# Performance work log

Hardware: AMD Instinct MI355X
Metric: run time of the kernel (lower is better)

Reference implementation:

```python
import jax, jax.numpy as jnp
import numpy as np

B, MAXLEN = 256, 10000
N_ATOMS, N_BONDS, N_ANG, N_TOR = 2000, 1999, 1998, 1997
NBT, NAT, NTT = 50, 100, 200
EPS = 1e-8


def setup_inputs() -> dict:
    rng = np.random.default_rng(0)
    feats = np.zeros((B, MAXLEN, 9), np.float32)
    # col 0: atom types
    feats[:, :N_ATOMS, 0] = rng.integers(0, 20, (B, N_ATOMS))
    # col 5: flattened coords [3*N]
    coords = (rng.standard_normal((B, N_ATOMS, 3)) * 2.0).astype(np.float32)
    feats[:, :3 * N_ATOMS, 5] = coords.reshape(B, -1)
    # col 6: bonds (i, j, type) along a chain
    i = np.arange(N_BONDS, dtype=np.float32)
    bonds = np.zeros((B, N_BONDS, 3), np.float32)
    bonds[..., 0] = i; bonds[..., 1] = i + 1
    bonds[..., 2] = rng.integers(0, NBT, (B, N_BONDS))
    feats[:, :3 * N_BONDS, 6] = bonds.reshape(B, -1)
    # col 7: angles (i, j, k, type)
    a = np.arange(N_ANG, dtype=np.float32)
    angs = np.zeros((B, N_ANG, 4), np.float32)
    angs[..., 0] = a; angs[..., 1] = a + 1; angs[..., 2] = a + 2
    angs[..., 3] = rng.integers(0, NAT, (B, N_ANG))
    feats[:, :4 * N_ANG, 7] = angs.reshape(B, -1)
    # col 8: torsions (i, j, k, l, type)
    t = np.arange(N_TOR, dtype=np.float32)
    tors = np.zeros((B, N_TOR, 5), np.float32)
    tors[..., 0] = t; tors[..., 1] = t + 1; tors[..., 2] = t + 2; tors[..., 3] = t + 3
    tors[..., 4] = rng.integers(0, NTT, (B, N_TOR))
    feats[:, :5 * N_TOR, 8] = tors.reshape(B, -1)
    # per-column valid lengths
    lengths = np.zeros((B, 9), np.int32)
    lengths[:, 0] = N_ATOMS
    lengths[:, 5] = 3 * N_ATOMS
    lengths[:, 6] = 3 * N_BONDS
    lengths[:, 7] = 4 * N_ANG
    lengths[:, 8] = 5 * N_TOR
    # learned params: (k, eq_value, multiplicity) per type row
    P = NBT + NAT + NTT
    opt = np.abs(rng.standard_normal((P, 3))).astype(np.float32)
    opt[:, 2] = rng.integers(1, 4, P).astype(np.float32)
    return {
        "features": jnp.asarray(feats),
        "lengths": jnp.asarray(lengths),
        "opt_pars": jnp.asarray(opt),
        "bond_type": jnp.arange(NBT, dtype=jnp.float32),
        "angle_type": jnp.arange(NAT, dtype=jnp.float32) + NBT,
        "tor_type": jnp.arange(NTT, dtype=jnp.float32) + NBT + NAT,
    }


def _gather(coords, idx):
    # coords [B,N,3], idx [B,M] -> [B,M,3]
    return jnp.take_along_axis(
        coords, jnp.broadcast_to(idx[..., None], idx.shape + (3,)), axis=1)


def _energy(features, lengths, opt_pars, bond_map, angle_map, tor_map):
    Bn = features.shape[0]
    coords = features[:, :3 * N_ATOMS, 5].reshape(Bn, N_ATOMS, 3)
    bonds = features[:, :3 * N_BONDS, 6].reshape(Bn, N_BONDS, 3).astype(jnp.int32)
    angs = features[:, :4 * N_ANG, 7].reshape(Bn, N_ANG, 4).astype(jnp.int32)
    tors = features[:, :5 * N_TOR, 8].reshape(Bn, N_TOR, 5).astype(jnp.int32)

    # ---- bonds: harmonic E = k * (r - r0)^2 ----
    ri, rj = _gather(coords, bonds[..., 0]), _gather(coords, bonds[..., 1])
    r = jnp.sqrt(jnp.sum((ri - rj) ** 2, -1) + EPS)          # [B,NB]
    pb = opt_pars[bond_map[bonds[..., 2]]]                   # [B,NB,3]
    eb = pb[..., 0] * (r - pb[..., 1]) ** 2
    mb = jnp.arange(N_BONDS)[None, :] < (lengths[:, 6:7] // 3)
    ebonds = jnp.sum(jnp.where(mb, eb, 0.0), -1)

    # ---- angles: harmonic E = k * (theta - theta0)^2 ----
    ai, aj, ak = (_gather(coords, angs[..., c]) for c in range(3))
    u, v = ai - aj, ak - aj
    cos = jnp.sum(u * v, -1) * jax.lax.rsqrt(
        (jnp.sum(u * u, -1) + EPS) * (jnp.sum(v * v, -1) + EPS))
    theta = jnp.arccos(jnp.clip(cos, -1.0 + 1e-6, 1.0 - 1e-6))
    pa = opt_pars[angle_map[angs[..., 3]]]
    ea = pa[..., 0] * (theta - pa[..., 1]) ** 2
    ma = jnp.arange(N_ANG)[None, :] < (lengths[:, 7:8] // 4)
    eangles = jnp.sum(jnp.where(ma, ea, 0.0), -1)

    # ---- torsions: E = k * (1 + cos(n*phi - phi0)) ----
    ti, tj, tk, tl = (_gather(coords, tors[..., c]) for c in range(4))
    b1, b2, b3 = tj - ti, tk - tj, tl - tk
    n1 = jnp.cross(b1, b2)
    n2 = jnp.cross(b2, b3)
    b2h = b2 * jax.lax.rsqrt(jnp.sum(b2 * b2, -1, keepdims=True) + EPS)
    m1 = jnp.cross(n1, b2h)
    phi = jnp.arctan2(jnp.sum(m1 * n2, -1), jnp.sum(n1 * n2, -1))
    pt = opt_pars[tor_map[tors[..., 4]]]
    et = pt[..., 0] * (1.0 + jnp.cos(pt[..., 2] * phi - pt[..., 1]))
    mt = jnp.arange(N_TOR)[None, :] < (lengths[:, 8:9] // 5)
    etors = jnp.sum(jnp.where(mt, et, 0.0), -1)

    return ebonds + eangles + etors                          # [B]


def reference(features, lengths, opt_pars, bond_type, angle_type, tor_type):
    return _energy(features, lengths, opt_pars,
                   bond_type.astype(jnp.int32),
                   angle_type.astype(jnp.int32),
                   tor_type.astype(jnp.int32))
```

## Files before the change

kernel.cpp:

```cpp
#include <hip/hip_runtime.h>


#define BS 512

__global__ __launch_bounds__(BS) void energy_kernel(
    const float* __restrict__ features,
    const int*   __restrict__ lengths,
    const float* __restrict__ opt_pars,
    const float* __restrict__ bond_type,
    const float* __restrict__ angle_type,
    const float* __restrict__ tor_type,
    float*       __restrict__ out)
{
    constexpr int MAXLEN  = 10000;
    constexpr int N_ATOMS = 2000;
    constexpr int NBT = 50, NAT = 100, NTT = 200;
    constexpr float EPS = 1e-8f;

    const int b   = blockIdx.x;
    const int tid = threadIdx.x;
    const float* __restrict__ fb = features + (size_t)b * MAXLEN * 9;

    __shared__ float sc[3 * N_ATOMS];
    __shared__ float sbp[3 * NBT];
    __shared__ float sap[3 * NAT];
    __shared__ float stp[3 * NTT];
    __shared__ float swsum[BS / 64];

    for (int i = tid; i < 3 * N_ATOMS; i += BS)
        sc[i] = fb[i * 9 + 5];

    for (int i = tid; i < NBT; i += BS) {
        int idx = (int)bond_type[i];
        sbp[3*i+0] = opt_pars[3*idx+0];
        sbp[3*i+1] = opt_pars[3*idx+1];
        sbp[3*i+2] = opt_pars[3*idx+2];
    }
    for (int i = tid; i < NAT; i += BS) {
        int idx = (int)angle_type[i];
        sap[3*i+0] = opt_pars[3*idx+0];
        sap[3*i+1] = opt_pars[3*idx+1];
        sap[3*i+2] = opt_pars[3*idx+2];
    }
    for (int i = tid; i < NTT; i += BS) {
        int idx = (int)tor_type[i];
        stp[3*i+0] = opt_pars[3*idx+0];
        stp[3*i+1] = opt_pars[3*idx+1];
        stp[3*i+2] = opt_pars[3*idx+2];
    }
    __syncthreads();

    float acc = 0.0f;

    {
        const int nb = lengths[b * 9 + 6] / 3;
        const float* __restrict__ c6 = fb + 6;
        for (int t = tid; t < nb; t += BS) {
            const int base = 27 * t;
            int i  = (int)c6[base];
            int j  = (int)c6[base + 9];
            int ty = (int)c6[base + 18];
            float dx = sc[3*i+0] - sc[3*j+0];
            float dy = sc[3*i+1] - sc[3*j+1];
            float dz = sc[3*i+2] - sc[3*j+2];
            float r  = sqrtf(dx*dx + dy*dy + dz*dz + EPS);
            float k  = sbp[3*ty+0];
            float d  = r - sbp[3*ty+1];
            acc += k * d * d;
        }
    }

    {
        const int na = lengths[b * 9 + 7] / 4;
        const float* __restrict__ c7 = fb + 7;
        for (int t = tid; t < na; t += BS) {
            const int base = 36 * t;
            int i  = (int)c7[base];
            int j  = (int)c7[base + 9];
            int k_ = (int)c7[base + 18];
            int ty = (int)c7[base + 27];
            float jx = sc[3*j+0], jy = sc[3*j+1], jz = sc[3*j+2];
            float ux = sc[3*i+0] - jx, uy = sc[3*i+1] - jy, uz = sc[3*i+2] - jz;
            float vx = sc[3*k_+0] - jx, vy = sc[3*k_+1] - jy, vz = sc[3*k_+2] - jz;
            float uv = ux*vx + uy*vy + uz*vz;
            float uu = ux*ux + uy*uy + uz*uz;
            float vv = vx*vx + vy*vy + vz*vz;
            float c  = uv * rsqrtf((uu + EPS) * (vv + EPS));
            c = fminf(fmaxf(c, -1.0f + 1e-6f), 1.0f - 1e-6f);
            float theta = acosf(c);
            float k  = sap[3*ty+0];
            float d  = theta - sap[3*ty+1];
            acc += k * d * d;
        }
    }

    {
        const int nt = lengths[b * 9 + 8] / 5;
        const float* __restrict__ c8 = fb + 8;
        for (int t = tid; t < nt; t += BS) {
            const int base = 45 * t;
            int i  = (int)c8[base];
            int j  = (int)c8[base + 9];
            int k_ = (int)c8[base + 18];
            int l  = (int)c8[base + 27];
            int ty = (int)c8[base + 36];
            float ix = sc[3*i+0],  iy = sc[3*i+1],  iz = sc[3*i+2];
            float jx = sc[3*j+0],  jy = sc[3*j+1],  jz = sc[3*j+2];
            float kx = sc[3*k_+0], ky = sc[3*k_+1], kz = sc[3*k_+2];
            float lx = sc[3*l+0],  ly = sc[3*l+1],  lz = sc[3*l+2];
            float b1x = jx - ix, b1y = jy - iy, b1z = jz - iz;
            float b2x = kx - jx, b2y = ky - jy, b2z = kz - jz;
            float b3x = lx - kx, b3y = ly - ky, b3z = lz - kz;
            float n1x = b1y*b2z - b1z*b2y;
            float n1y = b1z*b2x - b1x*b2z;
            float n1z = b1x*b2y - b1y*b2x;
            float n2x = b2y*b3z - b2z*b3y;
            float n2y = b2z*b3x - b2x*b3z;
            float n2z = b2x*b3y - b2y*b3x;
            float inv = rsqrtf(b2x*b2x + b2y*b2y + b2z*b2z + EPS);
            float hx = b2x * inv, hy = b2y * inv, hz = b2z * inv;
            float m1x = n1y*hz - n1z*hy;
            float m1y = n1z*hx - n1x*hz;
            float m1z = n1x*hy - n1y*hx;
            float sy = m1x*n2x + m1y*n2y + m1z*n2z;
            float sx = n1x*n2x + n1y*n2y + n1z*n2z;
            float phi = atan2f(sy, sx);
            float k  = stp[3*ty+0];
            float p0 = stp[3*ty+1];
            float n  = stp[3*ty+2];
            acc += k * (1.0f + cosf(n * phi - p0));
        }
    }

    for (int off = 32; off > 0; off >>= 1)
        acc += __shfl_down(acc, off, 64);
    const int wave = tid >> 6, lane = tid & 63;
    if (lane == 0) swsum[wave] = acc;
    __syncthreads();
    if (tid == 0) {
        float s = 0.0f;
        #pragma unroll
        for (int w = 0; w < BS / 64; ++w) s += swsum[w];
        out[b] = s;
    }
}

extern "C" void kernel_launch(void* const* d_in, const int* in_sizes, int n_in,
                              void* d_out, int out_size, void* d_ws, size_t ws_size,
                              hipStream_t stream) {
    const float* features   = (const float*)d_in[0];
    const int*   lengths    = (const int*)  d_in[1];
    const float* opt_pars   = (const float*)d_in[2];
    const float* bond_type  = (const float*)d_in[3];
    const float* angle_type = (const float*)d_in[4];
    const float* tor_type   = (const float*)d_in[5];
    float* out = (float*)d_out;

    const int B = out_size;
    energy_kernel<<<B, BS, 0, stream>>>(features, lengths, opt_pars,
                                        bond_type, angle_type, tor_type, out);
}
```

Measured before the change: 161.3 us.

## Stage all feature columns into LDS via coalesced float4 loads with u16 indices

Instead of strided scalar reads of the coordinate and index columns, each block streams its entire feature slab as float4 and scatters columns 5-8 into shared memory. Index columns are stored as 16-bit integers so the compute loops read compactly from LDS. This trades reading the unused columns and extra per-element div/branch work for fully coalesced global loads. It also uses much more dynamic shared memory, which may limit occupancy.

```diff
diff --git a/kernel.cpp b/kernel.cpp
--- a/kernel.cpp
+++ b/kernel.cpp
@@ -2,6 +2,21 @@
 
 
 #define BS 512
+
+constexpr int MAXLEN  = 10000;
+constexpr int N_ATOMS = 2000;
+constexpr int NBT = 50, NAT = 100, NTT = 200;
+constexpr float EPS = 1e-8f;
+
+constexpr int OFF_SC  = 0;
+constexpr int OFF_SBP = OFF_SC  + 6000 * 4;
+constexpr int OFF_SAP = OFF_SBP + 150 * 4;
+constexpr int OFF_STP = OFF_SAP + 300 * 4;
+constexpr int OFF_SW  = OFF_STP + 600 * 4;
+constexpr int OFF_SB  = OFF_SW  + 16 * 4;
+constexpr int OFF_SA  = OFF_SB  + 6000 * 2;
+constexpr int OFF_ST  = OFF_SA  + 8000 * 2;
+constexpr int SMEM_BYTES = OFF_ST + 9988 * 2;
 
 __global__ __launch_bounds__(BS) void energy_kernel(
     const float* __restrict__ features,
@@ -12,23 +27,18 @@
     const float* __restrict__ tor_type,
     float*       __restrict__ out)
 {
-    constexpr int MAXLEN  = 10000;
-    constexpr int N_ATOMS = 2000;
-    constexpr int NBT = 50, NAT = 100, NTT = 200;
-    constexpr float EPS = 1e-8f;
+    extern __shared__ char smem[];
+    float*          sc  = (float*)(smem + OFF_SC);
+    float*          sbp = (float*)(smem + OFF_SBP);
+    float*          sap = (float*)(smem + OFF_SAP);
+    float*          stp = (float*)(smem + OFF_STP);
+    float*          sw  = (float*)(smem + OFF_SW);
+    unsigned short* sb  = (unsigned short*)(smem + OFF_SB);
+    unsigned short* sa  = (unsigned short*)(smem + OFF_SA);
+    unsigned short* st  = (unsigned short*)(smem + OFF_ST);
 
     const int b   = blockIdx.x;
     const int tid = threadIdx.x;
-    const float* __restrict__ fb = features + (size_t)b * MAXLEN * 9;
-
-    __shared__ float sc[3 * N_ATOMS];
-    __shared__ float sbp[3 * NBT];
-    __shared__ float sap[3 * NAT];
-    __shared__ float stp[3 * NTT];
-    __shared__ float swsum[BS / 64];
-
-    for (int i = tid; i < 3 * N_ATOMS; i += BS)
-        sc[i] = fb[i * 9 + 5];
 
     for (int i = tid; i < NBT; i += BS) {
         int idx = (int)bond_type[i];
@@ -48,18 +58,39 @@
         stp[3*i+1] = opt_pars[3*idx+1];
         stp[3*i+2] = opt_pars[3*idx+2];
     }
+
+    const float4* __restrict__ fv =
+        (const float4*)(features + (size_t)b * MAXLEN * 9);
+
+    auto put = [&](unsigned g, float val) {
+        unsigned i   = g / 9u;
+        unsigned col = g - 9u * i;
+        if (col == 5u)      { if (i < 6000u) sc[i] = val; }
+        else if (col == 6u) { if (i < 5997u) sb[i] = (unsigned short)(int)val; }
+        else if (col == 7u) { if (i < 7992u) sa[i] = (unsigned short)(int)val; }
+        else if (col == 8u) { if (i < 9985u) st[i] = (unsigned short)(int)val; }
+    };
+
+    constexpr int NV = MAXLEN * 9 / 4;
+    #pragma unroll 4
+    for (int q = tid; q < NV; q += BS) {
+        float4 v = fv[q];
+        unsigned g0 = 4u * (unsigned)q;
+        put(g0 + 0u, v.x);
+        put(g0 + 1u, v.y);
+        put(g0 + 2u, v.z);
+        put(g0 + 3u, v.w);
+    }
     __syncthreads();
 
     float acc = 0.0f;
 
     {
         const int nb = lengths[b * 9 + 6] / 3;
-        const float* __restrict__ c6 = fb + 6;
         for (int t = tid; t < nb; t += BS) {
-            const int base = 27 * t;
-            int i  = (int)c6[base];
-            int j  = (int)c6[base + 9];
-            int ty = (int)c6[base + 18];
+            int i  = sb[3*t+0];
+            int j  = sb[3*t+1];
+            int ty = sb[3*t+2];
             float dx = sc[3*i+0] - sc[3*j+0];
             float dy = sc[3*i+1] - sc[3*j+1];
             float dz = sc[3*i+2] - sc[3*j+2];
@@ -72,13 +103,11 @@
 
     {
         const int na = lengths[b * 9 + 7] / 4;
-        const float* __restrict__ c7 = fb + 7;
         for (int t = tid; t < na; t += BS) {
-            const int base = 36 * t;
-            int i  = (int)c7[base];
-            int j  = (int)c7[base + 9];
-            int k_ = (int)c7[base + 18];
-            int ty = (int)c7[base + 27];
+            int i  = sa[4*t+0];
+            int j  = sa[4*t+1];
+            int k_ = sa[4*t+2];
+            int ty = sa[4*t+3];
             float jx = sc[3*j+0], jy = sc[3*j+1], jz = sc[3*j+2];
             float ux = sc[3*i+0] - jx, uy = sc[3*i+1] - jy, uz = sc[3*i+2] - jz;
             float vx = sc[3*k_+0] - jx, vy = sc[3*k_+1] - jy, vz = sc[3*k_+2] - jz;
@@ -96,14 +125,12 @@
 
     {
         const int nt = lengths[b * 9 + 8] / 5;
-        const float* __restrict__ c8 = fb + 8;
         for (int t = tid; t < nt; t += BS) {
-            const int base = 45 * t;
-            int i  = (int)c8[base];
-            int j  = (int)c8[base + 9];
-            int k_ = (int)c8[base + 18];
-            int l  = (int)c8[base + 27];
-            int ty = (int)c8[base + 36];
+            int i  = st[5*t+0];
+            int j  = st[5*t+1];
+            int k_ = st[5*t+2];
+            int l  = st[5*t+3];
+            int ty = st[5*t+4];
             float ix = sc[3*i+0],  iy = sc[3*i+1],  iz = sc[3*i+2];
             float jx = sc[3*j+0],  jy = sc[3*j+1],  jz = sc[3*j+2];
             float kx = sc[3*k_+0], ky = sc[3*k_+1], kz = sc[3*k_+2];
@@ -135,12 +162,12 @@
     for (int off = 32; off > 0; off >>= 1)
         acc += __shfl_down(acc, off, 64);
     const int wave = tid >> 6, lane = tid & 63;
-    if (lane == 0) swsum[wave] = acc;
+    if (lane == 0) sw[wave] = acc;
     __syncthreads();
     if (tid == 0) {
         float s = 0.0f;
         #pragma unroll
-        for (int w = 0; w < BS / 64; ++w) s += swsum[w];
+        for (int w = 0; w < BS / 64; ++w) s += sw[w];
         out[b] = s;
     }
 }
@@ -156,7 +183,11 @@
     const float* tor_type   = (const float*)d_in[5];
     float* out = (float*)d_out;
 
+    hipFuncSetAttribute((const void*)energy_kernel,
+                        hipFuncAttributeMaxDynamicSharedMemorySize, SMEM_BYTES);
+
     const int B = out_size;
-    energy_kernel<<<B, BS, 0, stream>>>(features, lengths, opt_pars,
-                                        bond_type, angle_type, tor_type, out);
+    energy_kernel<<<B, BS, SMEM_BYTES, stream>>>(features, lengths, opt_pars,
+                                                 bond_type, angle_type,
+                                                 tor_type, out);
 }
```

After: 190.8 us. 18.2% more time.

## Split each batch across multiple blocks and reduce partial sums in second kernel

Applied to the files above, without the earlier changes.

Each batch item is now handled by eight blocks of 256 threads, each covering a slice of the bond, angle and torsion lists, instead of one 512-thread block. A second small kernel sums the per-slice partials into the output. This raises the number of blocks in flight to fill the GPU better. In exchange, every slice block reloads the full coordinate table into shared memory, adding redundant strided global reads and an extra kernel launch.

```diff
diff --git a/kernel.cpp b/kernel.cpp
--- a/kernel.cpp
+++ b/kernel.cpp
@@ -1,34 +1,34 @@
 #include <hip/hip_runtime.h>
 
 
-#define BS 512
+#define BS 256
+#define NSLICE 8
 
-__global__ __launch_bounds__(BS) void energy_kernel(
+constexpr int MAXLEN  = 10000;
+constexpr int N_ATOMS = 2000;
+constexpr int NBT = 50, NAT = 100, NTT = 200;
+constexpr float EPS = 1e-8f;
+
+__global__ __launch_bounds__(BS) void energy_slice_kernel(
     const float* __restrict__ features,
     const int*   __restrict__ lengths,
     const float* __restrict__ opt_pars,
     const float* __restrict__ bond_type,
     const float* __restrict__ angle_type,
     const float* __restrict__ tor_type,
-    float*       __restrict__ out)
+    float*       __restrict__ ws)
 {
-    constexpr int MAXLEN  = 10000;
-    constexpr int N_ATOMS = 2000;
-    constexpr int NBT = 50, NAT = 100, NTT = 200;
-    constexpr float EPS = 1e-8f;
-
-    const int b   = blockIdx.x;
-    const int tid = threadIdx.x;
-    const float* __restrict__ fb = features + (size_t)b * MAXLEN * 9;
-
     __shared__ float sc[3 * N_ATOMS];
     __shared__ float sbp[3 * NBT];
     __shared__ float sap[3 * NAT];
     __shared__ float stp[3 * NTT];
-    __shared__ float swsum[BS / 64];
+    __shared__ float sw[BS / 64];
 
-    for (int i = tid; i < 3 * N_ATOMS; i += BS)
-        sc[i] = fb[i * 9 + 5];
+    const int blk = blockIdx.x;
+    const int b   = blk >> 3;
+    const int s   = blk & (NSLICE - 1);
+    const int tid = threadIdx.x;
+    const float* __restrict__ fb = features + (size_t)b * MAXLEN * 9;
 
     for (int i = tid; i < NBT; i += BS) {
         int idx = (int)bond_type[i];
@@ -48,14 +48,19 @@
         stp[3*i+1] = opt_pars[3*idx+1];
         stp[3*i+2] = opt_pars[3*idx+2];
     }
+
+    #pragma unroll 4
+    for (int i = tid; i < 3 * N_ATOMS; i += BS)
+        sc[i] = fb[i * 9 + 5];
     __syncthreads();
 
     float acc = 0.0f;
 
     {
         const int nb = lengths[b * 9 + 6] / 3;
+        const int t0 = (nb * s) / NSLICE, t1 = (nb * (s + 1)) / NSLICE;
         const float* __restrict__ c6 = fb + 6;
-        for (int t = tid; t < nb; t += BS) {
+        for (int t = t0 + tid; t < t1; t += BS) {
             const int base = 27 * t;
             int i  = (int)c6[base];
             int j  = (int)c6[base + 9];
@@ -72,8 +77,9 @@
 
     {
         const int na = lengths[b * 9 + 7] / 4;
+        const int t0 = (na * s) / NSLICE, t1 = (na * (s + 1)) / NSLICE;
         const float* __restrict__ c7 = fb + 7;
-        for (int t = tid; t < na; t += BS) {
+        for (int t = t0 + tid; t < t1; t += BS) {
             const int base = 36 * t;
             int i  = (int)c7[base];
             int j  = (int)c7[base + 9];
@@ -96,8 +102,9 @@
 
     {
         const int nt = lengths[b * 9 + 8] / 5;
+        const int t0 = (nt * s) / NSLICE, t1 = (nt * (s + 1)) / NSLICE;
         const float* __restrict__ c8 = fb + 8;
-        for (int t = tid; t < nt; t += BS) {
+        for (int t = t0 + tid; t < t1; t += BS) {
             const int base = 45 * t;
             int i  = (int)c8[base];
             int j  = (int)c8[base + 9];
@@ -135,13 +142,25 @@
     for (int off = 32; off > 0; off >>= 1)
         acc += __shfl_down(acc, off, 64);
     const int wave = tid >> 6, lane = tid & 63;
-    if (lane == 0) swsum[wave] = acc;
+    if (lane == 0) sw[wave] = acc;
     __syncthreads();
     if (tid == 0) {
-        float s = 0.0f;
+        float v = 0.0f;
         #pragma unroll
-        for (int w = 0; w < BS / 64; ++w) s += swsum[w];
-        out[b] = s;
+        for (int w = 0; w < BS / 64; ++w) v += sw[w];
+        ws[blk] = v;
+    }
+}
+
+__global__ __launch_bounds__(256) void reduce_kernel(
+    const float* __restrict__ ws, float* __restrict__ out, int B)
+{
+    int b = blockIdx.x * 256 + threadIdx.x;
+    if (b < B) {
+        float v = 0.0f;
+        #pragma unroll
+        for (int i = 0; i < NSLICE; ++i) v += ws[b * NSLICE + i];
+        out[b] = v;
     }
 }
 
@@ -155,8 +174,10 @@
     const float* angle_type = (const float*)d_in[4];
     const float* tor_type   = (const float*)d_in[5];
     float* out = (float*)d_out;
+    float* ws  = (float*)d_ws;
 
     const int B = out_size;
-    energy_kernel<<<B, BS, 0, stream>>>(features, lengths, opt_pars,
-                                        bond_type, angle_type, tor_type, out);
+    energy_slice_kernel<<<B * NSLICE, BS, 0, stream>>>(
+        features, lengths, opt_pars, bond_type, angle_type, tor_type, ws);
+    reduce_kernel<<<(B + 255) / 256, 256, 0, stream>>>(ws, out, B);
 }
```

Result: slower. 202.7 us (+25.6%).
